# Performance work log

Hardware: AMD Instinct MI355X
Metric: run time of the kernel (lower is better)

The kernel has to match this reference:

```python
import jax, jax.numpy as jnp
import numpy as np

BN_EPS = 1e-5


def setup_inputs() -> dict:
    key = jax.random.key(0)
    ks = jax.random.split(key, 11)
    B, C, Ci, D, H, W = 2, 256, 128, 8, 32, 32
    s = 0.02  # weight init scale
    return {
        "x": jax.random.normal(ks[0], (B, C, D, H, W), dtype=jnp.float32),
        "Wt": jax.random.normal(ks[1], (Ci, C), dtype=jnp.float32) * s,
        "bt": jax.random.normal(ks[2], (Ci,), dtype=jnp.float32) * s,
        "Wp": jax.random.normal(ks[3], (Ci, C), dtype=jnp.float32) * s,
        "bp": jax.random.normal(ks[4], (Ci,), dtype=jnp.float32) * s,
        "Wg": jax.random.normal(ks[5], (Ci, C), dtype=jnp.float32) * s,
        "bg": jax.random.normal(ks[6], (Ci,), dtype=jnp.float32) * s,
        "Ww": jax.random.normal(ks[7], (C, Ci), dtype=jnp.float32) * s,
        "bw": jax.random.normal(ks[8], (C,), dtype=jnp.float32) * s,
        "gamma": jax.random.normal(ks[9], (C,), dtype=jnp.float32),
        "beta": jax.random.normal(ks[10], (C,), dtype=jnp.float32),
    }


def reference(x, Wt, bt, Wp, bp, Wg, bg, Ww, bw, gamma, beta):
    # x: [B, C, D, H, W]; 1x1x1 Conv3d == per-position channel GEMM.
    B, C, D, H, W = x.shape
    xf = x.reshape(B, C, -1)  # [B, C, N], N = D*H*W

    theta = jnp.einsum('oc,bcn->bno', Wt, xf) + bt          # [B, N, Ci]
    phi = jnp.einsum('oc,bcn->bon', Wp, xf) + bp[None, :, None]  # [B, Ci, N]
    g = jnp.einsum('oc,bcn->bno', Wg, xf) + bg              # [B, N, Ci]

    # Unscaled, unmasked full self-attention over all N spatial positions.
    f = jnp.einsum('bnc,bcm->bnm', theta, phi)              # [B, N, N]
    a = jax.nn.softmax(f, axis=-1)
    y = jnp.einsum('bnm,bmc->bcn', a, g)                    # [B, Ci, N]

    # Output projection W: conv1x1 then BatchNorm3d (training-mode batch stats).
    wy = jnp.einsum('oc,bcn->bon', Ww, y) + bw[None, :, None]  # [B, C, N]
    mean = jnp.mean(wy, axis=(0, 2), keepdims=True)
    var = jnp.var(wy, axis=(0, 2), keepdims=True)
    wy_bn = (wy - mean) * jax.lax.rsqrt(var + BN_EPS)
    wy_bn = wy_bn * gamma[None, :, None] + beta[None, :, None]

    return wy_bn.reshape(B, C, D, H, W) + x
```

## Files before the change

kernel.cpp:

```cpp
#include <hip/hip_runtime.h>
#include <cstdint>
#include <cstddef>


typedef unsigned short u16;
typedef __bf16 bf16x8 __attribute__((ext_vector_type(8)));
typedef float f32x4 __attribute__((ext_vector_type(4)));
typedef float f32x16 __attribute__((ext_vector_type(16)));
typedef unsigned short u16x8 __attribute__((ext_vector_type(8)));

#define B_ 2
#define C_ 256
#define CI_ 128
#define N_ 8192
#define KVB 64

static __device__ __forceinline__ u16 f2bf(float f){
  unsigned u = __builtin_bit_cast(unsigned, f);
  unsigned r = (u + 0x7FFFu + ((u>>16)&1u)) >> 16;
  return (u16)r;
}
static __device__ __forceinline__ float bf2f(u16 v){
  unsigned u = ((unsigned)v) << 16;
  return __builtin_bit_cast(float, u);
}
static __device__ __forceinline__ f32x4 f4zero(){
  f32x4 v; v[0]=0.f; v[1]=0.f; v[2]=0.f; v[3]=0.f; return v;
}
static __device__ __forceinline__ f32x16 f16zero(){
  f32x16 v;
#pragma unroll
  for (int i=0;i<16;i++) v[i]=0.f;
  return v;
}
static __device__ __forceinline__ f32x4 mfma16(bf16x8 a, bf16x8 b, f32x4 c){
  return __builtin_amdgcn_mfma_f32_16x16x32_bf16(a, b, c, 0, 0, 0);
}
static __device__ __forceinline__ f32x16 mfma32(bf16x8 a, bf16x8 b, f32x16 c){
  return __builtin_amdgcn_mfma_f32_32x32x16_bf16(a, b, c, 0, 0, 0);
}
static __device__ __forceinline__ unsigned cvtpk(float lo, float hi){
  unsigned r;
  asm("v_cvt_pk_bf16_f32 %0, %1, %2" : "=v"(r) : "v"(lo), "v"(hi));
  return r;
}
static __device__ __forceinline__ void plswap(unsigned &a, unsigned &b){
  asm volatile("v_permlane32_swap_b32 %0, %1" : "+v"(a), "+v"(b));
}

#define LOG2E 1.4426950408889634f

__global__ void k0_prep(const float* __restrict__ Wt, const float* __restrict__ Wp,
                        const float* __restrict__ Wg, const float* __restrict__ Ww,
                        const float* __restrict__ bt, const float* __restrict__ bp,
                        const float* __restrict__ bg,
                        u16* __restrict__ Wcat, u16* __restrict__ Wwb,
                        float* __restrict__ biasc, float* __restrict__ stats){
  int t = blockIdx.x*blockDim.x + threadIdx.x;
  int nthr = gridDim.x*blockDim.x;
  for (int i = t; i < 32768; i += nthr){
    Wcat[i]        = f2bf(Wt[i] * LOG2E);
    Wcat[32768+i]  = f2bf(Wp[i]);
    Wcat[65536+i]  = f2bf(Wg[i]);
    Wwb[i]         = f2bf(Ww[i]);
  }
  for (int i = t; i < 128; i += nthr){
    biasc[i] = bt[i] * LOG2E; biasc[128+i] = bp[i]; biasc[256+i] = bg[i];
  }
  for (int i = t; i < 512; i += nthr) stats[i] = 0.f;
}

__global__ __launch_bounds__(256) void k1_proj(const float* __restrict__ x,
     const u16* __restrict__ Wcat, const float* __restrict__ biasc,
     u16* __restrict__ theta, u16* __restrict__ kproj, u16* __restrict__ gT){
  __shared__ u16 At[64*264];
  __shared__ u16 Wt_[32*264];
  __shared__ u16 gbuf[32*72];
  int tid = threadIdx.x;
  int b  = blockIdx.x >> 7;
  int nb = (blockIdx.x & 127) * 64;
  int w = tid >> 6, lane = tid & 63;
  int l15 = lane & 15, kg = lane >> 4;

  {
    int cp = tid & 127, nh = tid >> 7;
    int c0 = cp*2;
    const float* src0 = x + ((size_t)(b*C_ + c0))*N_ + nb + nh*32;
    const float* src1 = src0 + N_;
#pragma unroll
    for (int j=0;j<8;j++){
      f32x4 a = *(const f32x4*)(src0 + j*4);
      f32x4 c = *(const f32x4*)(src1 + j*4);
#pragma unroll
      for (int q=0;q<4;q++){
        unsigned pk = (unsigned)f2bf(a[q]) | ((unsigned)f2bf(c[q])<<16);
        *(unsigned*)&At[(nh*32 + j*4 + q)*264 + c0] = pk;
      }
    }
  }
  __syncthreads();

  bf16x8 afr[8];
#pragma unroll
  for (int kc=0;kc<8;kc++)
    afr[kc] = *(const bf16x8*)&At[(w*16+l15)*264 + kc*32 + kg*8];

  for (int och = 0; och < 12; och++){
    {
      int o8 = tid>>3, cp8 = tid&7;
      const u16* wsrc = Wcat + ((size_t)(och*32 + o8))*256 + cp8*8;
#pragma unroll
      for (int j=0;j<4;j++)
        *(u16x8*)&Wt_[o8*264 + cp8*8 + j*64] = *(const u16x8*)(wsrc + j*64);
    }
    __syncthreads();

    f32x4 acc0 = f4zero(), acc1 = f4zero();
#pragma unroll
    for (int kc=0;kc<8;kc++){
      bf16x8 b0 = *(const bf16x8*)&Wt_[(l15)*264 + kc*32 + kg*8];
      bf16x8 b1 = *(const bf16x8*)&Wt_[(16+l15)*264 + kc*32 + kg*8];
      acc0 = mfma16(afr[kc], b0, acc0);
      acc1 = mfma16(afr[kc], b1, acc1);
    }

    if (och < 8){
      u16* dst = (och < 4) ? theta : kproj;
      int oo = (och & 3) * 32;
#pragma unroll
      for (int of=0;of<2;of++){
        int o = oo + of*16 + l15;
        float bias = biasc[och*32 + of*16 + l15];
        f32x4 acc = of ? acc1 : acc0;
#pragma unroll
        for (int i=0;i<4;i++){
          int n = nb + w*16 + kg*4 + i;
          dst[((size_t)b*N_ + n)*CI_ + o] = f2bf(acc[i] + bias);
        }
      }
      __syncthreads();
    } else {
#pragma unroll
      for (int of=0;of<2;of++){
        int o = of*16 + l15;
        float bias = biasc[och*32 + of*16 + l15];
        f32x4 acc = of ? acc1 : acc0;
#pragma unroll
        for (int i=0;i<4;i++){
          int r = w*16 + kg*4 + i;
          gbuf[o*72 + r] = f2bf(acc[i] + bias);
        }
      }
      __syncthreads();
      {
        int o = tid>>3, np = tid&7;
        int og = (och-8)*32 + o;
        u16x8 v = *(const u16x8*)&gbuf[o*72 + np*8];
        *(u16x8*)(gT + ((size_t)b*CI_ + og)*N_ + nb + np*8) = v;
      }
      __syncthreads();
    }
  }
}

__global__ __launch_bounds__(256, 2) void k2_attn(const u16* __restrict__ theta,
      const u16* __restrict__ kproj, const u16* __restrict__ gT,
      u16* __restrict__ pO, float* __restrict__ pM, float* __restrict__ pL){
  constexpr int CHUNK_N = 2048;
  constexpr int NTI = CHUNK_N / KVB;
  __shared__ char smem[65536];
  char* kbase = smem;
  char* vbase = smem + 32768;
  int tid = threadIdx.x;
  int bid = blockIdx.x;
  int combo = bid & 7;
  int b = combo & 1;
  int chunk = combo >> 1;
  int qblk = bid >> 3;
  int n0 = chunk * CHUNK_N;
  int w = tid >> 6, lane = tid & 63;
  int l31 = lane & 31, hi = lane >> 5;
  int qg = qblk*128 + w*32 + l31;

  bf16x8 qf[8];
  {
    const u16* qsrc = theta + ((size_t)b*N_ + qg)*CI_ + hi*8;
#pragma unroll
    for (int cc=0; cc<8; cc++) qf[cc] = *(const bf16x8*)(qsrc + cc*16);
  }

  int krow_s = tid >> 2, kpart = tid & 3;
  int vrow_s = tid >> 1, vpart = tid & 1;
  const u16* ksrc = kproj + ((size_t)b*N_ + n0 + krow_s)*CI_ + kpart*32;
  const u16* vsrc = gT + ((size_t)b*CI_ + vrow_s)*N_ + n0 + vpart*32;
  int kw_off[4], vw_off[4];
#pragma unroll
  for (int j=0;j<4;j++){
    kw_off[j] = krow_s*256 + ((kpart*64 + j*16) ^ ((krow_s&7)<<4));
    vw_off[j] = vrow_s*128 + ((vpart*64 + j*16) ^ ((vrow_s&7)<<4));
  }
  int swz = (l31&7)<<4;
  int kro[8], vro[4];
#pragma unroll
  for (int cc=0;cc<8;cc++) kro[cc] = l31*256 + ((cc*32 + hi*16) ^ swz);
#pragma unroll
  for (int ks=0;ks<4;ks++) vro[ks] = l31*128 + ((ks*32 + hi*16) ^ swz);

#pragma unroll
  for (int j=0;j<4;j++) *(u16x8*)(kbase + kw_off[j]) = *(const u16x8*)(ksrc + j*8);
#pragma unroll
  for (int j=0;j<4;j++) *(u16x8*)(vbase + vw_off[j]) = *(const u16x8*)(vsrc + j*8);
  __syncthreads();

  f32x16 oacc[4];
#pragma unroll
  for (int i=0;i<4;i++) oacc[i] = f16zero();
  float mrun = -1e30f, lrun = 0.f;

  for (int t=0; t<NTI; t++){
    int cur = t & 1;
    char* kb_c = kbase + cur*16384;
    char* vb_c = vbase + cur*16384;
    u16x8 kst[4], vst[4];
    bool pf = (t+1 < NTI);
    if (pf){
      const u16* ks = ksrc + (size_t)(t+1)*KVB*CI_;
      const u16* vs = vsrc + (t+1)*KVB;
#pragma unroll
      for (int j=0;j<4;j++) kst[j] = *(const u16x8*)(ks + j*8);
#pragma unroll
      for (int j=0;j<4;j++) vst[j] = *(const u16x8*)(vs + j*8);
    }

    f32x16 sA = f16zero(), sB = f16zero();
    __builtin_amdgcn_s_setprio(1);
#pragma unroll
    for (int cc=0; cc<8; cc++){
      bf16x8 kf0 = *(const bf16x8*)(kb_c + kro[cc]);
      bf16x8 kf1 = *(const bf16x8*)(kb_c + 8192 + kro[cc]);
      sA = mfma32(kf0, qf[cc], sA);
      sB = mfma32(kf1, qf[cc], sB);
    }
    __builtin_amdgcn_s_setprio(0);

    float t8[8];
#pragma unroll
    for (int i=0;i<8;i++) t8[i] = fmaxf(fmaxf(sA[i], sA[i+8]), fmaxf(sB[i], sB[i+8]));
    float m4a = fmaxf(t8[0], t8[4]), m4b = fmaxf(t8[1], t8[5]);
    float m4c = fmaxf(t8[2], t8[6]), m4d = fmaxf(t8[3], t8[7]);
    float mx = fmaxf(fmaxf(m4a, m4b), fmaxf(m4c, m4d));
    mx = fmaxf(mx, __shfl_xor(mx, 32));
    if (__any(mx > mrun + 12.f)){
      float mnew = fmaxf(mrun, mx);
      float sc = exp2f(mrun - mnew);
      lrun *= sc;
#pragma unroll
      for (int i=0;i<4;i++)
#pragma unroll
        for (int r=0;r<16;r++) oacc[i][r] *= sc;
      mrun = mnew;
    }
    float pA[16], pB[16];
#pragma unroll
    for (int r=0;r<16;r++){ pA[r] = exp2f(sA[r]-mrun); pB[r] = exp2f(sB[r]-mrun); }
    float s8[8];
#pragma unroll
    for (int i=0;i<8;i++) s8[i] = (pA[i]+pA[i+8]) + (pB[i]+pB[i+8]);
    float s4a = s8[0]+s8[4], s4b = s8[1]+s8[5], s4c = s8[2]+s8[6], s4d = s8[3]+s8[7];
    float ps = (s4a+s4b) + (s4c+s4d);
    ps += __shfl_xor(ps, 32);
    lrun += ps;

    if (pf){
      char* kd = kbase + (cur^1)*16384;
      char* vd = vbase + (cur^1)*16384;
#pragma unroll
      for (int j=0;j<4;j++) *(u16x8*)(kd + kw_off[j]) = kst[j];
#pragma unroll
      for (int j=0;j<4;j++) *(u16x8*)(vd + vw_off[j]) = vst[j];
    }

    __builtin_amdgcn_s_setprio(1);
#pragma unroll
    for (int ks=0; ks<4; ks++){
      const float* P = (ks<2) ? pA : pB;
      int r0 = (ks&1)*8;
      unsigned a0 = cvtpk(P[r0+0], P[r0+1]);
      unsigned b0 = cvtpk(P[r0+4], P[r0+5]);
      unsigned a1 = cvtpk(P[r0+2], P[r0+3]);
      unsigned b1 = cvtpk(P[r0+6], P[r0+7]);
      plswap(a0, b0); plswap(a1, b1);
      union { unsigned u[4]; bf16x8 v; } pb;
      pb.u[0]=a0; pb.u[1]=a1; pb.u[2]=b0; pb.u[3]=b1;
#pragma unroll
      for (int c2=0; c2<4; c2++){
        bf16x8 vf = *(const bf16x8*)(vb_c + c2*4096 + vro[ks]);
        oacc[c2] = mfma32(vf, pb.v, oacc[c2]);
      }
    }
    __builtin_amdgcn_s_setprio(0);
    __syncthreads();
  }

  char* region = smem + w*8192;
#pragma unroll
  for (int c2=0;c2<4;c2++)
#pragma unroll
    for (int r=0;r<16;r++){
      int c = c2*32 + (r&3) + 8*(r>>2) + 4*hi;
      *(u16*)(region + l31*256 + ((c*2) ^ swz)) = f2bf(oacc[c2][r]);
    }
  __syncthreads();
  {
    int ql = lane >> 1, half = lane & 1;
    int qg2 = qblk*128 + w*32 + ql;
    u16* dst = pO + ((size_t)(chunk*2 + b)*N_ + qg2)*CI_ + half*64;
    int rswz = (ql&7)<<4;
#pragma unroll
    for (int j=0;j<8;j++){
      u16x8 v2 = *(const u16x8*)(region + ql*256 + ((half*128 + j*16) ^ rswz));
      *(u16x8*)(dst + j*8) = v2;
    }
  }
  if (hi == 0){
    pM[(size_t)(chunk*2 + b)*N_ + qg] = mrun;
    pL[(size_t)(chunk*2 + b)*N_ + qg] = lrun;
  }
}

__global__ __launch_bounds__(256) void k3_wy(const u16* __restrict__ pO,
    const float* __restrict__ pM, const float* __restrict__ pL,
    const u16* __restrict__ Wwb, const float* __restrict__ bw,
    u16* __restrict__ wy, float* __restrict__ stats){
  __shared__ u16 Yt[64*136];
  __shared__ u16 Wt_[64*136];
  __shared__ float wyb[64*72];
  int tid = threadIdx.x;
  int b  = blockIdx.x >> 7;
  int nb = (blockIdx.x & 127) * 64;
  int w = tid>>6, lane = tid&63;
  int l15 = lane&15, kg = lane>>4;

  {
    int n = tid>>2, cp = tid&3;
    size_t q = (size_t)nb + n;
    float m[4], l[4];
#pragma unroll
    for (int ch=0; ch<4; ch++){
      m[ch] = pM[(size_t)(ch*2+b)*N_ + q];
      l[ch] = pL[(size_t)(ch*2+b)*N_ + q];
    }
    float M = fmaxf(fmaxf(m[0],m[1]), fmaxf(m[2],m[3]));
    float wts[4]; float L = 0.f;
#pragma unroll
    for (int ch=0; ch<4; ch++){ wts[ch] = exp2f(m[ch]-M); L += wts[ch]*l[ch]; }
    float inv = 1.f/L;
#pragma unroll
    for (int j=0;j<4;j++){
      int c0 = cp*32 + j*8;
      float acc[8];
#pragma unroll
      for (int i=0;i<8;i++) acc[i]=0.f;
#pragma unroll
      for (int ch=0; ch<4; ch++){
        u16x8 v = *(const u16x8*)(pO + ((size_t)(ch*2+b)*N_ + q)*CI_ + c0);
#pragma unroll
        for (int i=0;i<8;i++) acc[i] += wts[ch]*bf2f(v[i]);
      }
#pragma unroll
      for (int i=0;i<4;i++){
        unsigned pk = (unsigned)f2bf(acc[2*i]*inv) | ((unsigned)f2bf(acc[2*i+1]*inv)<<16);
        *(unsigned*)&Yt[n*136 + c0 + 2*i] = pk;
      }
    }
  }
  __syncthreads();

  bf16x8 afr[4];
#pragma unroll
  for (int kc=0;kc<4;kc++)
    afr[kc] = *(const bf16x8*)&Yt[(w*16+l15)*136 + kc*32 + kg*8];

  for (int oc=0; oc<4; oc++){
    {
      int o = tid>>2, cp = tid&3;
      const u16* src = Wwb + ((size_t)(oc*64 + o))*CI_ + cp*32;
#pragma unroll
      for (int j=0;j<4;j++)
        *(u16x8*)&Wt_[o*136 + cp*32 + j*8] = *(const u16x8*)(src + j*8);
    }
    __syncthreads();

    f32x4 acc[4];
#pragma unroll
    for (int of=0;of<4;of++) acc[of] = f4zero();
#pragma unroll
    for (int kc=0;kc<4;kc++){
#pragma unroll
      for (int of=0;of<4;of++){
        bf16x8 bfr = *(const bf16x8*)&Wt_[(of*16+l15)*136 + kc*32 + kg*8];
        acc[of] = mfma16(afr[kc], bfr, acc[of]);
      }
    }
#pragma unroll
    for (int of=0;of<4;of++){
#pragma unroll
      for (int i=0;i<4;i++)
        wyb[(of*16+l15)*72 + w*16 + kg*4 + i] = acc[of][i];
    }
    __syncthreads();
    {
      int o = tid>>2, np = tid&3;
      int og = oc*64 + o;
      float bias = bw[og];
      float sm = 0.f, sq = 0.f;
      u16* dst = wy + ((size_t)b*C_ + og)*N_ + nb + np*16;
      u16 buf[16];
#pragma unroll
      for (int j=0;j<4;j++){
#pragma unroll
        for (int q2=0;q2<4;q2++){
          float t2 = wyb[o*72 + np*16 + j*4 + q2] + bias;
          buf[j*4+q2] = f2bf(t2); sm += t2; sq += t2*t2;
        }
      }
      *(u16x8*)dst = *(const u16x8*)&buf[0];
      *(u16x8*)(dst+8) = *(const u16x8*)&buf[8];
      sm += __shfl_xor(sm, 1); sm += __shfl_xor(sm, 2);
      sq += __shfl_xor(sq, 1); sq += __shfl_xor(sq, 2);
      if ((tid&3)==0){
        atomicAdd(&stats[og], sm);
        atomicAdd(&stats[256+og], sq);
      }
    }
    __syncthreads();
  }
}

__global__ __launch_bounds__(256) void k4_bn(const u16* __restrict__ wy,
    const float* __restrict__ x, const float* __restrict__ stats,
    const float* __restrict__ gamma, const float* __restrict__ beta,
    float* __restrict__ out){
  size_t base = ((size_t)blockIdx.x)*2048 + (size_t)threadIdx.x*8;
  int o = (int)((base >> 13) & 255);
  const float invn = 1.f/16384.f;
  float mean = stats[o]*invn;
  float var  = stats[256+o]*invn - mean*mean;
  float rs = rsqrtf(var + 1e-5f);
  float g = gamma[o]*rs;
  float bb = beta[o];
  u16x8 a = *(const u16x8*)(wy + base);
  f32x4 x0 = *(const f32x4*)(x + base);
  f32x4 x1 = *(const f32x4*)(x + base + 4);
  f32x4 r0, r1;
#pragma unroll
  for (int q=0;q<4;q++){
    r0[q] = (bf2f(a[q])-mean)*g + bb + x0[q];
    r1[q] = (bf2f(a[4+q])-mean)*g + bb + x1[q];
  }
  *(f32x4*)(out + base)     = r0;
  *(f32x4*)(out + base + 4) = r1;
}

extern "C" void kernel_launch(void* const* d_in, const int* in_sizes, int n_in,
                              void* d_out, int out_size, void* d_ws, size_t ws_size,
                              hipStream_t stream){
  const float* x     = (const float*)d_in[0];
  const float* Wt    = (const float*)d_in[1];
  const float* bt    = (const float*)d_in[2];
  const float* Wp    = (const float*)d_in[3];
  const float* bp    = (const float*)d_in[4];
  const float* Wg    = (const float*)d_in[5];
  const float* bg    = (const float*)d_in[6];
  const float* Ww    = (const float*)d_in[7];
  const float* bw    = (const float*)d_in[8];
  const float* gamma = (const float*)d_in[9];
  const float* beta  = (const float*)d_in[10];

  char* ws = (char*)d_ws;
  u16*   theta = (u16*)(ws + 0);
  u16*   kproj = (u16*)(ws + 4194304);
  u16*   gT    = (u16*)(ws + 8388608);
  u16*   pO    = (u16*)(ws + 12582912);
  float* pM    = (float*)(ws + 29360128);
  float* pL    = (float*)(ws + 29622272);
  u16*   wy    = (u16*)(ws + 29884416);
  u16*   Wcat  = (u16*)(ws + 38273024);
  u16*   Wwb   = (u16*)(ws + 38469632);
  float* biasc = (float*)(ws + 38535168);
  float* stats = (float*)(ws + 38536704);
  float* out   = (float*)d_out;

  k0_prep<<<64, 256, 0, stream>>>(Wt, Wp, Wg, Ww, bt, bp, bg, Wcat, Wwb, biasc, stats);
  k1_proj<<<256, 256, 0, stream>>>(x, Wcat, biasc, theta, kproj, gT);
  k2_attn<<<512, 256, 0, stream>>>(theta, kproj, gT, pO, pM, pL);
  k3_wy<<<256, 256, 0, stream>>>(pO, pM, pL, Wwb, bw, wy, stats);
  k4_bn<<<2048, 256, 0, stream>>>(wy, x, stats, gamma, beta, out);
}
```

Baseline: 145.6 us.

## Use direct global-to-LDS loads and 512-thread attention blocks sharing K/V tiles

The attention kernel now stages K and V tiles with global_load_lds, which writes straight into shared memory instead of going through registers and explicit LDS stores. The XOR swizzle moves from the LDS write address to the global read address. Blocks double to 512 threads covering 256 queries, so each K/V tile loaded into LDS is reused by twice as many query rows, and the grid is halved. The risks are the register budget under the new launch bounds and whether the async LDS writes are waited on correctly before the barrier.

```diff
diff --git a/kernel.cpp b/kernel.cpp
--- a/kernel.cpp
+++ b/kernel.cpp
@@ -46,6 +46,10 @@
 }
 static __device__ __forceinline__ void plswap(unsigned &a, unsigned &b){
   asm volatile("v_permlane32_swap_b32 %0, %1" : "+v"(a), "+v"(b));
+}
+static __device__ __forceinline__ void glds16(const void* g, void* l){
+  __builtin_amdgcn_global_load_lds((const __attribute__((address_space(1))) void*)g,
+                                   (__attribute__((address_space(3))) void*)l, 16, 0, 0);
 }
 
 #define LOG2E 1.4426950408889634f
@@ -163,7 +167,7 @@
   }
 }
 
-__global__ __launch_bounds__(256, 2) void k2_attn(const u16* __restrict__ theta,
+__global__ __launch_bounds__(512, 2) void k2_attn(const u16* __restrict__ theta,
       const u16* __restrict__ kproj, const u16* __restrict__ gT,
       u16* __restrict__ pO, float* __restrict__ pM, float* __restrict__ pL){
   constexpr int CHUNK_N = 2048;
@@ -180,7 +184,7 @@
   int n0 = chunk * CHUNK_N;
   int w = tid >> 6, lane = tid & 63;
   int l31 = lane & 31, hi = lane >> 5;
-  int qg = qblk*128 + w*32 + l31;
+  int qg = qblk*256 + w*32 + l31;
 
   bf16x8 qf[8];
   {
@@ -189,16 +193,15 @@
     for (int cc=0; cc<8; cc++) qf[cc] = *(const bf16x8*)(qsrc + cc*16);
   }
 
-  int krow_s = tid >> 2, kpart = tid & 3;
-  int vrow_s = tid >> 1, vpart = tid & 1;
-  const u16* ksrc = kproj + ((size_t)b*N_ + n0 + krow_s)*CI_ + kpart*32;
-  const u16* vsrc = gT + ((size_t)b*CI_ + vrow_s)*N_ + n0 + vpart*32;
-  int kw_off[4], vw_off[4];
-#pragma unroll
-  for (int j=0;j<4;j++){
-    kw_off[j] = krow_s*256 + ((kpart*64 + j*16) ^ ((krow_s&7)<<4));
-    vw_off[j] = vrow_s*128 + ((vpart*64 + j*16) ^ ((vrow_s&7)<<4));
-  }
+  int kr = w*4 + (lane>>4);
+  int kcol = ((lane&15)*16) ^ ((kr&7)<<4);
+  const char* kg_base = (const char*)kproj + ((size_t)b*N_ + n0 + kr)*256 + kcol;
+  char* kd_base = kbase + w*1024;
+  int vr = w*8 + (lane>>3);
+  int vcol = ((lane&7)*16) ^ ((vr&7)<<4);
+  const char* vg_base = (const char*)gT + (((size_t)b*CI_ + vr)*N_ + n0)*2 + vcol;
+  char* vd_base = vbase + w*1024;
+
   int swz = (l31&7)<<4;
   int kro[8], vro[4];
 #pragma unroll
@@ -206,10 +209,10 @@
 #pragma unroll
   for (int ks=0;ks<4;ks++) vro[ks] = l31*128 + ((ks*32 + hi*16) ^ swz);
 
-#pragma unroll
-  for (int j=0;j<4;j++) *(u16x8*)(kbase + kw_off[j]) = *(const u16x8*)(ksrc + j*8);
-#pragma unroll
-  for (int j=0;j<4;j++) *(u16x8*)(vbase + vw_off[j]) = *(const u16x8*)(vsrc + j*8);
+  glds16(kg_base, kd_base);
+  glds16(kg_base + 8192, kd_base + 8192);
+  glds16(vg_base, vd_base);
+  glds16(vg_base + (size_t)64*N_*2, vd_base + 8192);
   __syncthreads();
 
   f32x16 oacc[4];
@@ -221,15 +224,16 @@
     int cur = t & 1;
     char* kb_c = kbase + cur*16384;
     char* vb_c = vbase + cur*16384;
-    u16x8 kst[4], vst[4];
-    bool pf = (t+1 < NTI);
-    if (pf){
-      const u16* ks = ksrc + (size_t)(t+1)*KVB*CI_;
-      const u16* vs = vsrc + (t+1)*KVB;
-#pragma unroll
-      for (int j=0;j<4;j++) kst[j] = *(const u16x8*)(ks + j*8);
-#pragma unroll
-      for (int j=0;j<4;j++) vst[j] = *(const u16x8*)(vs + j*8);
+
+    if (t+1 < NTI){
+      const char* kg = kg_base + (size_t)(t+1)*16384;
+      const char* vg = vg_base + (size_t)(t+1)*128;
+      char* kd = kd_base + (cur^1)*16384;
+      char* vd = vd_base + (cur^1)*16384;
+      glds16(kg, kd);
+      glds16(kg + 8192, kd + 8192);
+      glds16(vg, vd);
+      glds16(vg + (size_t)64*N_*2, vd + 8192);
     }
 
     f32x16 sA = f16zero(), sB = f16zero();
@@ -270,15 +274,6 @@
     float ps = (s4a+s4b) + (s4c+s4d);
     ps += __shfl_xor(ps, 32);
     lrun += ps;
-
-    if (pf){
-      char* kd = kbase + (cur^1)*16384;
-      char* vd = vbase + (cur^1)*16384;
-#pragma unroll
-      for (int j=0;j<4;j++) *(u16x8*)(kd + kw_off[j]) = kst[j];
-#pragma unroll
-      for (int j=0;j<4;j++) *(u16x8*)(vd + vw_off[j]) = vst[j];
-    }
 
     __builtin_amdgcn_s_setprio(1);
 #pragma unroll
@@ -313,7 +308,7 @@
   __syncthreads();
   {
     int ql = lane >> 1, half = lane & 1;
-    int qg2 = qblk*128 + w*32 + ql;
+    int qg2 = qblk*256 + w*32 + ql;
     u16* dst = pO + ((size_t)(chunk*2 + b)*N_ + qg2)*CI_ + half*64;
     int rswz = (ql&7)<<4;
 #pragma unroll
@@ -493,7 +488,7 @@
 
   k0_prep<<<64, 256, 0, stream>>>(Wt, Wp, Wg, Ww, bt, bp, bg, Wcat, Wwb, biasc, stats);
   k1_proj<<<256, 256, 0, stream>>>(x, Wcat, biasc, theta, kproj, gT);
-  k2_attn<<<512, 256, 0, stream>>>(theta, kproj, gT, pO, pM, pL);
+  k2_attn<<<256, 512, 0, stream>>>(theta, kproj, gT, pO, pM, pL);
   k3_wy<<<256, 256, 0, stream>>>(pO, pM, pL, Wwb, bw, wy, stats);
   k4_bn<<<2048, 256, 0, stream>>>(wy, x, stats, gamma, beta, out);
 }
```

After: 142.9 us. About the same (-1.9%).
